# Performance work log

Measured on AMD Instinct MI355X. Metric: run time of the kernel, lower is better.

The kernel has to match this reference:

```python
import jax, jax.numpy as jnp
import numpy as np

NUM_USERS = 100000
NUM_ITEMS = 50000
EMBED_DIM = 128
NNZ = 2000000
N_LAYERS = 3


def setup_inputs() -> dict:
    key = jax.random.key(0)
    k1, k2, k3, k4, k5 = jax.random.split(key, 5)
    stdv = 1.0 / np.sqrt(EMBED_DIM)
    user_pref = jax.random.uniform(k1, (NUM_USERS, EMBED_DIM), jnp.float32, -stdv, stdv)
    item_pref = jax.random.uniform(k2, (NUM_ITEMS, EMBED_DIM), jnp.float32, -stdv, stdv)
    vals = jax.random.uniform(k3, (NNZ,), jnp.float32)
    rows = jax.random.randint(k4, (NNZ,), 0, NUM_USERS, jnp.int32)
    cols = jax.random.randint(k5, (NNZ,), 0, NUM_ITEMS, jnp.int32)
    return {"user_pref": user_pref, "item_pref": item_pref, "vals": vals,
            "rows": rows, "cols": cols}


def _spmm(vals, src_idx, dst_idx, x, num_out):
    # y[dst] += vals * x[src]  — SpMM over COO edge list
    msgs = vals[:, None] * x[src_idx]            # [nnz, D]
    return jax.ops.segment_sum(msgs, dst_idx, num_segments=num_out)


def reference(user_pref, item_pref, vals, rows, cols):
    u, it = user_pref, item_pref
    u_sum, i_sum = user_pref, item_pref
    for _ in range(N_LAYERS):
        # u_next = Graph @ item_layer ; i_next = Graph.T @ user_layer (same layer index)
        u_next = _spmm(vals, cols, rows, it, NUM_USERS)   # [U, D]
        i_next = _spmm(vals, rows, cols, u, NUM_ITEMS)    # [I, D]
        u, it = u_next, i_next
        u_sum = u_sum + u
        i_sum = i_sum + it
    inv = 1.0 / (N_LAYERS + 1)
    return (u_sum * inv, i_sum * inv)
```

## Files before the change

### kernel.cpp

```cpp
#include <hip/hip_runtime.h>


#define NUM_USERS 100000
#define NUM_ITEMS 50000
#define EMBED_DIM 128
#define NNZ_COUNT 2000000
#define NBUCK_U 391
#define NBUCK_I 196
#define EPB 8192
#define NBLK 245

typedef float v2f __attribute__((ext_vector_type(2)));


__device__ __forceinline__ unsigned bf16_rnd(float f) {
    unsigned u = __float_as_uint(f);
    return (u + 0x7FFFu + ((u >> 16) & 1u)) >> 16;
}
__device__ __forceinline__ unsigned pack_bf16(float x, float y) {
    return bf16_rnd(x) | (bf16_rnd(y) << 16);
}

__global__ __launch_bounds__(256) void to_bf16_dual(
    const float* __restrict__ a, unsigned* __restrict__ oa, int na8,
    const float* __restrict__ b, unsigned* __restrict__ ob, int nb8)
{
    int i = blockIdx.x * 256 + threadIdx.x;
    const float4* s4; uint4* d4;
    if (i < na8) {
        s4 = reinterpret_cast<const float4*>(a) + i * 2;
        d4 = reinterpret_cast<uint4*>(oa) + i;
    } else {
        i -= na8;
        if (i >= nb8) return;
        s4 = reinterpret_cast<const float4*>(b) + i * 2;
        d4 = reinterpret_cast<uint4*>(ob) + i;
    }
    float4 x = s4[0], y = s4[1];
    uint4 r;
    r.x = pack_bf16(x.x, x.y); r.y = pack_bf16(x.z, x.w);
    r.z = pack_bf16(y.x, y.y); r.w = pack_bf16(y.z, y.w);
    *d4 = r;
}


__global__ __launch_bounds__(256) void msplit_hist(
    const int* __restrict__ rows, const int* __restrict__ cols,
    int* __restrict__ hist_u, int* __restrict__ hist_i)
{
    __shared__ int h[NBUCK_U + NBUCK_I];
    for (int i = threadIdx.x; i < NBUCK_U + NBUCK_I; i += 256) h[i] = 0;
    __syncthreads();
    const int base = blockIdx.x * EPB;
    const int end = min(base + EPB, NNZ_COUNT);
    for (int e = base + threadIdx.x; e < end; e += 256) {
        atomicAdd(&h[rows[e] >> 8], 1);
        atomicAdd(&h[NBUCK_U + (cols[e] >> 8)], 1);
    }
    __syncthreads();
    for (int b = threadIdx.x; b < NBUCK_U; b += 256)
        hist_u[b * NBLK + blockIdx.x] = h[b];
    for (int b = threadIdx.x; b < NBUCK_I; b += 256)
        hist_i[b * NBLK + blockIdx.x] = h[NBUCK_U + b];
}

__global__ __launch_bounds__(256) void msplit_offsets(
    const int* __restrict__ hist_u, const int* __restrict__ hist_i,
    int* __restrict__ offs_u, int* __restrict__ offs_i,
    int* __restrict__ tot_u, int* __restrict__ tot_i)
{
    __shared__ int buf[256];
    int b = blockIdx.x;
    const int* hist; int* offs; int* tot; int nbuck;
    if (b < NBUCK_U) { hist = hist_u; offs = offs_u; tot = tot_u; nbuck = NBUCK_U; }
    else { b -= NBUCK_U; hist = hist_i; offs = offs_i; tot = tot_i; nbuck = NBUCK_I; }
    const int t = threadIdx.x;
    const int x = (t < NBLK) ? hist[b * NBLK + t] : 0;
    buf[t] = x;
    __syncthreads();
    for (int d = 1; d < 256; d <<= 1) {
        const int y = (t >= d) ? buf[t - d] : 0;
        __syncthreads();
        buf[t] += y;
        __syncthreads();
    }
    if (t < NBLK) offs[t * nbuck + b] = buf[t] - x;
    if (t == 255) tot[b] = buf[255];
}

__global__ __launch_bounds__(512) void scan_buckets(
    const int* __restrict__ tot_u, int* __restrict__ bbase_u,
    const int* __restrict__ tot_i, int* __restrict__ bbase_i)
{
    __shared__ int buf[512];
    const int t = threadIdx.x;
    const int* tot; int* bbase; int nb;
    if (blockIdx.x == 0) { tot = tot_u; bbase = bbase_u; nb = NBUCK_U; }
    else                 { tot = tot_i; bbase = bbase_i; nb = NBUCK_I; }
    const int v = (t < nb) ? tot[t] : 0;
    buf[t] = v;
    __syncthreads();
    for (int d = 1; d < 512; d <<= 1) {
        const int y = (t >= d) ? buf[t - d] : 0;
        __syncthreads();
        buf[t] += y;
        __syncthreads();
    }
    if (t <= nb) bbase[t] = buf[t] - v;
}

__global__ __launch_bounds__(256) void msplit_scatter(
    const int* __restrict__ rows, const int* __restrict__ cols,
    const float* __restrict__ vals,
    const int* __restrict__ offs_u, const int* __restrict__ offs_i,
    const int* __restrict__ bbase_u, const int* __restrict__ bbase_i,
    int2* __restrict__ stage_u, int2* __restrict__ stage_i)
{
    __shared__ int cu[NBUCK_U];
    __shared__ int ci[NBUCK_I];
    const int t = threadIdx.x;
    for (int b = t; b < NBUCK_U; b += 256)
        cu[b] = offs_u[blockIdx.x * NBUCK_U + b] + bbase_u[b];
    for (int b = t; b < NBUCK_I; b += 256)
        ci[b] = offs_i[blockIdx.x * NBUCK_I + b] + bbase_i[b];
    __syncthreads();
    const int base = blockIdx.x * EPB;
    const int end = min(base + EPB, NNZ_COUNT);
    for (int e = base + t; e < end; e += 256) {
        const int r = rows[e];
        const int c = cols[e];
        const int vb = __float_as_int(vals[e]);
        const int su = atomicAdd(&cu[r >> 8], 1);
        stage_u[su] = make_int2(c | ((r & 255) << 16), vb);
        const int si = atomicAdd(&ci[c >> 8], 1);
        stage_i[si] = make_int2(r | ((c & 255) << 17), vb);
    }
}

__global__ __launch_bounds__(256) void bucket_build(
    const int* __restrict__ bbase_u, const int2* __restrict__ stage_u,
    unsigned* __restrict__ pairs_u, int* __restrict__ ptr_u,
    const int* __restrict__ bbase_i, const int2* __restrict__ stage_i,
    unsigned* __restrict__ pairs_i, int* __restrict__ ptr_i)
{
    __shared__ int hcnt[256];
    __shared__ int buf[256];
    __shared__ int cur[256];
    const int t = threadIdx.x;
    int b = blockIdx.x;
    const bool uside = (b < NBUCK_U);
    const int* bbase; const int2* stage; unsigned* pairs; int* ptr; int n; int sh;
    if (uside) { bbase = bbase_u; stage = stage_u; pairs = pairs_u; ptr = ptr_u; n = NUM_USERS; sh = 16; }
    else { b -= NBUCK_U; bbase = bbase_i; stage = stage_i; pairs = pairs_i; ptr = ptr_i; n = NUM_ITEMS; sh = 17; }
    const int beg = bbase[b];
    const int end = bbase[b + 1];

    hcnt[t] = 0;
    __syncthreads();
    for (int idx = beg + t; idx < end; idx += 256)
        atomicAdd(&hcnt[(stage[idx].x >> sh) & 255], 1);
    __syncthreads();

    const int v = hcnt[t];
    buf[t] = v;
    __syncthreads();
    for (int d = 1; d < 256; d <<= 1) {
        const int y = (t >= d) ? buf[t - d] : 0;
        __syncthreads();
        buf[t] += y;
        __syncthreads();
    }
    const int rowbase = beg + buf[t] - v;
    cur[t] = rowbase;
    const int first = b << 8;
    if (first + t < n) ptr[first + t] = rowbase;
    if (first + t == n) ptr[n] = end;
    else if (first + 256 == n && t == 0) ptr[n] = end;
    __syncthreads();

    for (int idx = beg + t; idx < end; idx += 256) {
        const int2 s = stage[idx];
        const int local = (s.x >> sh) & 255;
        const unsigned vb = bf16_rnd(__int_as_float(s.y));
        unsigned packed;
        if (uside) packed = (unsigned)(s.x & 0xFFFF) | (vb << 16);
        else       packed = (unsigned)(s.x & 0x1FFFF) | ((vb & 0x7FFFu) << 17);
        const int slot = atomicAdd(&cur[local], 1);
        pairs[slot] = packed;
    }
}


template<bool USIDE>
__device__ __forceinline__ void decode_pair(unsigned s, int& c, float& v) {
    if (USIDE) { c = (int)(s & 0xFFFFu);  v = __uint_as_float(s & 0xFFFF0000u); }
    else       { c = (int)(s & 0x1FFFFu); v = __uint_as_float((s & 0xFFFE0000u) >> 1); }
}

template<int MODE, bool USIDE>
__device__ __forceinline__ void spmm_row_bf(
    const int* __restrict__ ptr, const unsigned* __restrict__ pairs,
    const unsigned* __restrict__ src, unsigned* __restrict__ dst,
    const unsigned* __restrict__ l1, const unsigned* __restrict__ l2,
    const float* __restrict__ base, float* __restrict__ out,
    int row, int lane)
{
    const int start = __builtin_amdgcn_readfirstlane(ptr[row]);
    const int end   = __builtin_amdgcn_readfirstlane(ptr[row + 1]);
    const unsigned* __restrict__ srcl = src + lane;
    v2f acc; acc.x = 0.f; acc.y = 0.f;

    int e = start;
    for (; e + 16 <= end; e += 16) {
        unsigned s[16]; int c[16]; float v[16]; unsigned g[16];
        #pragma unroll
        for (int k = 0; k < 16; ++k) s[k] = pairs[e + k];
        #pragma unroll
        for (int k = 0; k < 16; ++k) {
            decode_pair<USIDE>(s[k], c[k], v[k]);
            g[k] = srcl[(size_t)c[k] * 64];
        }
        #pragma unroll
        for (int k = 0; k < 16; ++k) {
            v2f gv; gv.x = __uint_as_float(g[k] << 16);
            gv.y = __uint_as_float(g[k] & 0xFFFF0000u);
            acc += v[k] * gv;
        }
    }
    for (; e + 8 <= end; e += 8) {
        unsigned s[8]; int c[8]; float v[8]; unsigned g[8];
        #pragma unroll
        for (int k = 0; k < 8; ++k) s[k] = pairs[e + k];
        #pragma unroll
        for (int k = 0; k < 8; ++k) {
            decode_pair<USIDE>(s[k], c[k], v[k]);
            g[k] = srcl[(size_t)c[k] * 64];
        }
        #pragma unroll
        for (int k = 0; k < 8; ++k) {
            v2f gv; gv.x = __uint_as_float(g[k] << 16);
            gv.y = __uint_as_float(g[k] & 0xFFFF0000u);
            acc += v[k] * gv;
        }
    }
    for (; e < end; ++e) {
        const unsigned s = pairs[e];
        int c; float v;
        decode_pair<USIDE>(s, c, v);
        const unsigned g = srcl[(size_t)c * 64];
        v2f gv; gv.x = __uint_as_float(g << 16);
        gv.y = __uint_as_float(g & 0xFFFF0000u);
        acc += v * gv;
    }

    if (MODE == 0) {
        __builtin_nontemporal_store(pack_bf16(acc.x, acc.y),
                                    dst + (size_t)row * 64 + lane);
    } else {
        const unsigned a1 = __builtin_nontemporal_load(l1 + (size_t)row * 64 + lane);
        const unsigned a2 = __builtin_nontemporal_load(l2 + (size_t)row * 64 + lane);
        const size_t o = (size_t)row * EMBED_DIM + (lane << 1);
        const v2f bs = __builtin_nontemporal_load(
            reinterpret_cast<const v2f*>(base + o));
        v2f r;
        r.x = (bs.x + __uint_as_float(a1 << 16) + __uint_as_float(a2 << 16) + acc.x) * 0.25f;
        r.y = (bs.y + __uint_as_float(a1 & 0xFFFF0000u) + __uint_as_float(a2 & 0xFFFF0000u) + acc.y) * 0.25f;
        __builtin_nontemporal_store(r, reinterpret_cast<v2f*>(out + o));
    }
}

template<int MODE>
__global__ __launch_bounds__(256) void csr_spmm_dual_bf(
    const int* __restrict__ ptr_u, const unsigned* __restrict__ pairs_u,
    const unsigned* __restrict__ src_u, unsigned* __restrict__ dst_u,
    const unsigned* __restrict__ l1_u, const unsigned* __restrict__ l2_u,
    const float* __restrict__ base_u, float* __restrict__ out_u,
    const int* __restrict__ ptr_i, const unsigned* __restrict__ pairs_i,
    const unsigned* __restrict__ src_i, unsigned* __restrict__ dst_i,
    const unsigned* __restrict__ l1_i, const unsigned* __restrict__ l2_i,
    const float* __restrict__ base_i, float* __restrict__ out_i,
    int GU)
{
    const int lane = threadIdx.x & 63;
    const int w = threadIdx.x >> 6;
    if ((int)blockIdx.x < GU) {
        const int row = blockIdx.x * 4 + w;
        if (row < NUM_USERS)
            spmm_row_bf<MODE, true>(ptr_u, pairs_u, src_u, dst_u, l1_u, l2_u, base_u, out_u, row, lane);
    } else {
        const int row = ((int)blockIdx.x - GU) * 4 + w;
        if (row < NUM_ITEMS)
            spmm_row_bf<MODE, false>(ptr_i, pairs_i, src_i, dst_i, l1_i, l2_i, base_i, out_i, row, lane);
    }
}


__global__ __launch_bounds__(256) void edge_spmm(
    const float* __restrict__ vals, const int* __restrict__ rows,
    const int* __restrict__ cols, const float* __restrict__ u_src,
    const float* __restrict__ i_src, float* __restrict__ u_dst,
    float* __restrict__ i_dst, int nnz)
{
    const int lane = threadIdx.x & 31;
    const int e = blockIdx.x * 8 + (threadIdx.x >> 5);
    if (e >= nnz) return;
    const float v = vals[e];
    const size_t ro = (size_t)rows[e] * EMBED_DIM + lane * 4;
    const size_t co = (size_t)cols[e] * EMBED_DIM + lane * 4;
    const float4 iv = *reinterpret_cast<const float4*>(i_src + co);
    const float4 uv = *reinterpret_cast<const float4*>(u_src + ro);
    atomicAdd(u_dst + ro + 0, v * iv.x); atomicAdd(u_dst + ro + 1, v * iv.y);
    atomicAdd(u_dst + ro + 2, v * iv.z); atomicAdd(u_dst + ro + 3, v * iv.w);
    atomicAdd(i_dst + co + 0, v * uv.x); atomicAdd(i_dst + co + 1, v * uv.y);
    atomicAdd(i_dst + co + 2, v * uv.z); atomicAdd(i_dst + co + 3, v * uv.w);
}

__global__ __launch_bounds__(256) void acc_scale(
    float* __restrict__ out, const float* __restrict__ x, long n, float scale)
{
    long i = ((long)blockIdx.x * blockDim.x + threadIdx.x) * 4;
    if (i >= n) return;
    float4 o = *reinterpret_cast<float4*>(out + i);
    float4 a = *reinterpret_cast<const float4*>(x + i);
    o.x = (o.x + a.x) * scale; o.y = (o.y + a.y) * scale;
    o.z = (o.z + a.z) * scale; o.w = (o.w + a.w) * scale;
    *reinterpret_cast<float4*>(out + i) = o;
}


extern "C" void kernel_launch(void* const* d_in, const int* in_sizes, int n_in,
                              void* d_out, int out_size, void* d_ws, size_t ws_size,
                              hipStream_t stream)
{
    const float* user = (const float*)d_in[0];
    const float* item = (const float*)d_in[1];
    const float* vals = (const float*)d_in[2];
    const int*   rows = (const int*)d_in[3];
    const int*   cols = (const int*)d_in[4];

    const size_t UD = (size_t)NUM_USERS * EMBED_DIM;
    const size_t ID = (size_t)NUM_ITEMS * EMBED_DIM;

    float* out_u = (float*)d_out;
    float* out_i = out_u + UD;

    char* ws = (char*)d_ws;
    unsigned* user_bf = (unsigned*)ws;              ws += UD * 2;
    unsigned* item_bf = (unsigned*)ws;              ws += ID * 2;
    unsigned* uA = (unsigned*)ws;                   ws += UD * 2;
    unsigned* uB = (unsigned*)ws;                   ws += UD * 2;
    unsigned* iA = (unsigned*)ws;                   ws += ID * 2;
    unsigned* iB = (unsigned*)ws;                   ws += ID * 2;
    unsigned* pairs_u = (unsigned*)ws;              ws += (size_t)NNZ_COUNT * 4;
    unsigned* pairs_i = (unsigned*)ws;              ws += (size_t)NNZ_COUNT * 4;
    int2* stage_u = (int2*)ws;                      ws += (size_t)NNZ_COUNT * 8;
    int2* stage_i = (int2*)ws;                      ws += (size_t)NNZ_COUNT * 8;
    int* ptr_u = (int*)ws;                          ws += (NUM_USERS + 1) * 4;
    int* ptr_i = (int*)ws;                          ws += (NUM_ITEMS + 1) * 4;
    int* bbase_u = (int*)ws;                        ws += (NBUCK_U + 1) * 4;
    int* bbase_i = (int*)ws;                        ws += (NBUCK_I + 1) * 4;
    const size_t REQ = (size_t)(ws - (char*)d_ws);

    int* hist_u = (int*)pairs_u;
    int* hist_i = hist_u + NBUCK_U * NBLK;
    int* offs_u = hist_i + NBUCK_I * NBLK;
    int* offs_i = offs_u + NBLK * NBUCK_U;
    int* tot_u  = offs_i + NBLK * NBUCK_I;
    int* tot_i  = tot_u + NBUCK_U;

    if (ws_size >= REQ) {
        const int NA8 = (int)(UD / 8), NB8 = (int)(ID / 8);
        to_bf16_dual<<<(NA8 + NB8 + 255) / 256, 256, 0, stream>>>(
            user, user_bf, NA8, item, item_bf, NB8);

        msplit_hist<<<NBLK, 256, 0, stream>>>(rows, cols, hist_u, hist_i);
        msplit_offsets<<<NBUCK_U + NBUCK_I, 256, 0, stream>>>(
            hist_u, hist_i, offs_u, offs_i, tot_u, tot_i);
        scan_buckets<<<2, 512, 0, stream>>>(tot_u, bbase_u, tot_i, bbase_i);
        msplit_scatter<<<NBLK, 256, 0, stream>>>(
            rows, cols, vals, offs_u, offs_i, bbase_u, bbase_i, stage_u, stage_i);
        bucket_build<<<NBUCK_U + NBUCK_I, 256, 0, stream>>>(
            bbase_u, stage_u, pairs_u, ptr_u,
            bbase_i, stage_i, pairs_i, ptr_i);

        const int GU = (NUM_USERS + 3) / 4;
        const int GI = (NUM_ITEMS + 3) / 4;

        csr_spmm_dual_bf<0><<<GU + GI, 256, 0, stream>>>(
            ptr_u, pairs_u, item_bf, uA, nullptr, nullptr, nullptr, nullptr,
            ptr_i, pairs_i, user_bf, iA, nullptr, nullptr, nullptr, nullptr, GU);
        csr_spmm_dual_bf<0><<<GU + GI, 256, 0, stream>>>(
            ptr_u, pairs_u, iA, uB, nullptr, nullptr, nullptr, nullptr,
            ptr_i, pairs_i, uA, iB, nullptr, nullptr, nullptr, nullptr, GU);
        csr_spmm_dual_bf<1><<<GU + GI, 256, 0, stream>>>(
            ptr_u, pairs_u, iB, nullptr, uA, uB, user, out_u,
            ptr_i, pairs_i, uB, nullptr, iA, iB, item, out_i, GU);
    } else {
        char* fw = (char*)d_ws;
        float* fuA = (float*)fw;                    fw += UD * 4;
        float* fuB = (float*)fw;                    fw += UD * 4;
        float* fiA = (float*)fw;                    fw += ID * 4;
        float* fiB = (float*)fw;                    fw += ID * 4;

        const int EDGE_BLOCKS = (NNZ_COUNT + 7) / 8;
        const int ACC_U = (int)(UD / 1024), ACC_I = (int)(ID / 1024);

        hipMemcpyAsync(out_u, user, UD * 4, hipMemcpyDeviceToDevice, stream);
        hipMemcpyAsync(out_i, item, ID * 4, hipMemcpyDeviceToDevice, stream);

        hipMemsetAsync(fuA, 0, UD * 4, stream);
        hipMemsetAsync(fiA, 0, ID * 4, stream);
        edge_spmm<<<EDGE_BLOCKS, 256, 0, stream>>>(vals, rows, cols, user, item, fuA, fiA, NNZ_COUNT);
        acc_scale<<<ACC_U, 256, 0, stream>>>(out_u, fuA, (long)UD, 1.0f);
        acc_scale<<<ACC_I, 256, 0, stream>>>(out_i, fiA, (long)ID, 1.0f);

        hipMemsetAsync(fuB, 0, UD * 4, stream);
        hipMemsetAsync(fiB, 0, ID * 4, stream);
        edge_spmm<<<EDGE_BLOCKS, 256, 0, stream>>>(vals, rows, cols, fuA, fiA, fuB, fiB, NNZ_COUNT);
        acc_scale<<<ACC_U, 256, 0, stream>>>(out_u, fuB, (long)UD, 1.0f);
        acc_scale<<<ACC_I, 256, 0, stream>>>(out_i, fiB, (long)ID, 1.0f);

        hipMemsetAsync(fuA, 0, UD * 4, stream);
        hipMemsetAsync(fiA, 0, ID * 4, stream);
        edge_spmm<<<EDGE_BLOCKS, 256, 0, stream>>>(vals, rows, cols, fuB, fiB, fuA, fiA, NNZ_COUNT);
        acc_scale<<<ACC_U, 256, 0, stream>>>(out_u, fuA, (long)UD, 0.25f);
        acc_scale<<<ACC_I, 256, 0, stream>>>(out_i, fiA, (long)ID, 0.25f);
    }
}
```

Before: 639.7 us.

## Stage scatter and bucket build through LDS for coalesced global writes

The multisplit scatter now sorts each block's edges by bucket in shared memory before writing them out, so writes to the staging arrays form contiguous runs instead of one random write per edge. The block size is halved to 4096 edges (489 blocks) and the offset scan is widened to 512 threads to match. bucket_build likewise assembles each bucket's packed pairs in an LDS buffer and writes them out contiguously when the bucket fits in BCAP entries, otherwise it falls back to direct scatter. This costs extra shared memory, more barriers, and a second pass over rows/cols per side. Preprocessing is only part of the total time, so the effect is bounded.

```diff
diff --git a/kernel.cpp b/kernel.cpp
--- a/kernel.cpp
+++ b/kernel.cpp
@@ -7,8 +7,9 @@
 #define NNZ_COUNT 2000000
 #define NBUCK_U 391
 #define NBUCK_I 196
-#define EPB 8192
-#define NBLK 245
+#define EPB 4096
+#define NBLK 489
+#define BCAP 12288
 
 typedef float v2f __attribute__((ext_vector_type(2)));
 
@@ -64,12 +65,12 @@
         hist_i[b * NBLK + blockIdx.x] = h[NBUCK_U + b];
 }
 
-__global__ __launch_bounds__(256) void msplit_offsets(
+__global__ __launch_bounds__(512) void msplit_offsets(
     const int* __restrict__ hist_u, const int* __restrict__ hist_i,
     int* __restrict__ offs_u, int* __restrict__ offs_i,
     int* __restrict__ tot_u, int* __restrict__ tot_i)
 {
-    __shared__ int buf[256];
+    __shared__ int buf[512];
     int b = blockIdx.x;
     const int* hist; int* offs; int* tot; int nbuck;
     if (b < NBUCK_U) { hist = hist_u; offs = offs_u; tot = tot_u; nbuck = NBUCK_U; }
@@ -78,14 +79,14 @@
     const int x = (t < NBLK) ? hist[b * NBLK + t] : 0;
     buf[t] = x;
     __syncthreads();
-    for (int d = 1; d < 256; d <<= 1) {
+    for (int d = 1; d < 512; d <<= 1) {
         const int y = (t >= d) ? buf[t - d] : 0;
         __syncthreads();
         buf[t] += y;
         __syncthreads();
     }
     if (t < NBLK) offs[t * nbuck + b] = buf[t] - x;
-    if (t == 255) tot[b] = buf[255];
+    if (t == 511) tot[b] = buf[511];
 }
 
 __global__ __launch_bounds__(512) void scan_buckets(
@@ -109,32 +110,95 @@
     if (t <= nb) bbase[t] = buf[t] - v;
 }
 
-__global__ __launch_bounds__(256) void msplit_scatter(
+__global__ __launch_bounds__(512) void msplit_scatter(
     const int* __restrict__ rows, const int* __restrict__ cols,
     const float* __restrict__ vals,
     const int* __restrict__ offs_u, const int* __restrict__ offs_i,
     const int* __restrict__ bbase_u, const int* __restrict__ bbase_i,
     int2* __restrict__ stage_u, int2* __restrict__ stage_i)
 {
-    __shared__ int cu[NBUCK_U];
-    __shared__ int ci[NBUCK_I];
+    __shared__ int buf[512];
+    __shared__ int cur[512];
+    __shared__ int gb[512];
+    __shared__ int ed0[EPB], ed1[EPB];
+    __shared__ unsigned short bpos[EPB];
     const int t = threadIdx.x;
-    for (int b = t; b < NBUCK_U; b += 256)
-        cu[b] = offs_u[blockIdx.x * NBUCK_U + b] + bbase_u[b];
-    for (int b = t; b < NBUCK_I; b += 256)
-        ci[b] = offs_i[blockIdx.x * NBUCK_I + b] + bbase_i[b];
-    __syncthreads();
     const int base = blockIdx.x * EPB;
     const int end = min(base + EPB, NNZ_COUNT);
-    for (int e = base + t; e < end; e += 256) {
+    const int n = end - base;
+
+    buf[t] = 0;
+    __syncthreads();
+    for (int e = base + t; e < end; e += 512)
+        atomicAdd(&buf[rows[e] >> 8], 1);
+    __syncthreads();
+    int x = buf[t];
+    __syncthreads();
+    {
+        buf[t] = x;
+        __syncthreads();
+        for (int d = 1; d < 512; d <<= 1) {
+            const int y = (t >= d) ? buf[t - d] : 0;
+            __syncthreads();
+            buf[t] += y;
+            __syncthreads();
+        }
+    }
+    {
+        const int excl = buf[t] - x;
+        cur[t] = excl;
+        if (t < NBUCK_U)
+            gb[t] = offs_u[blockIdx.x * NBUCK_U + t] + bbase_u[t] - excl;
+    }
+    __syncthreads();
+    for (int e = base + t; e < end; e += 512) {
         const int r = rows[e];
+        const int b = r >> 8;
+        const int pos = atomicAdd(&cur[b], 1);
+        ed0[pos] = cols[e] | ((r & 255) << 16);
+        ed1[pos] = __float_as_int(vals[e]);
+        bpos[pos] = (unsigned short)b;
+    }
+    __syncthreads();
+    for (int k = t; k < n; k += 512)
+        stage_u[gb[bpos[k]] + k] = make_int2(ed0[k], ed1[k]);
+    __syncthreads();
+
+    buf[t] = 0;
+    __syncthreads();
+    for (int e = base + t; e < end; e += 512)
+        atomicAdd(&buf[cols[e] >> 8], 1);
+    __syncthreads();
+    x = buf[t];
+    __syncthreads();
+    {
+        buf[t] = x;
+        __syncthreads();
+        for (int d = 1; d < 512; d <<= 1) {
+            const int y = (t >= d) ? buf[t - d] : 0;
+            __syncthreads();
+            buf[t] += y;
+            __syncthreads();
+        }
+    }
+    {
+        const int excl = buf[t] - x;
+        cur[t] = excl;
+        if (t < NBUCK_I)
+            gb[t] = offs_i[blockIdx.x * NBUCK_I + t] + bbase_i[t] - excl;
+    }
+    __syncthreads();
+    for (int e = base + t; e < end; e += 512) {
         const int c = cols[e];
-        const int vb = __float_as_int(vals[e]);
-        const int su = atomicAdd(&cu[r >> 8], 1);
-        stage_u[su] = make_int2(c | ((r & 255) << 16), vb);
-        const int si = atomicAdd(&ci[c >> 8], 1);
-        stage_i[si] = make_int2(r | ((c & 255) << 17), vb);
-    }
+        const int b = c >> 8;
+        const int pos = atomicAdd(&cur[b], 1);
+        ed0[pos] = rows[e] | ((c & 255) << 17);
+        ed1[pos] = __float_as_int(vals[e]);
+        bpos[pos] = (unsigned short)b;
+    }
+    __syncthreads();
+    for (int k = t; k < n; k += 512)
+        stage_i[gb[bpos[k]] + k] = make_int2(ed0[k], ed1[k]);
 }
 
 __global__ __launch_bounds__(256) void bucket_build(
@@ -146,6 +210,7 @@
     __shared__ int hcnt[256];
     __shared__ int buf[256];
     __shared__ int cur[256];
+    __shared__ unsigned plds[BCAP];
     const int t = threadIdx.x;
     int b = blockIdx.x;
     const bool uside = (b < NBUCK_U);
@@ -154,6 +219,7 @@
     else { b -= NBUCK_U; bbase = bbase_i; stage = stage_i; pairs = pairs_i; ptr = ptr_i; n = NUM_ITEMS; sh = 17; }
     const int beg = bbase[b];
     const int end = bbase[b + 1];
+    const int cnt = end - beg;
 
     hcnt[t] = 0;
     __syncthreads();
@@ -170,23 +236,42 @@
         buf[t] += y;
         __syncthreads();
     }
-    const int rowbase = beg + buf[t] - v;
-    cur[t] = rowbase;
+    const int excl = buf[t] - v;
+    const int rowbase = beg + excl;
     const int first = b << 8;
     if (first + t < n) ptr[first + t] = rowbase;
     if (first + t == n) ptr[n] = end;
     else if (first + 256 == n && t == 0) ptr[n] = end;
-    __syncthreads();
-
-    for (int idx = beg + t; idx < end; idx += 256) {
-        const int2 s = stage[idx];
-        const int local = (s.x >> sh) & 255;
-        const unsigned vb = bf16_rnd(__int_as_float(s.y));
-        unsigned packed;
-        if (uside) packed = (unsigned)(s.x & 0xFFFF) | (vb << 16);
-        else       packed = (unsigned)(s.x & 0x1FFFF) | ((vb & 0x7FFFu) << 17);
-        const int slot = atomicAdd(&cur[local], 1);
-        pairs[slot] = packed;
+
+    if (cnt <= BCAP) {
+        cur[t] = excl;
+        __syncthreads();
+        for (int idx = beg + t; idx < end; idx += 256) {
+            const int2 s = stage[idx];
+            const int local = (s.x >> sh) & 255;
+            const unsigned vb = bf16_rnd(__int_as_float(s.y));
+            unsigned packed;
+            if (uside) packed = (unsigned)(s.x & 0xFFFF) | (vb << 16);
+            else       packed = (unsigned)(s.x & 0x1FFFF) | ((vb & 0x7FFFu) << 17);
+            const int slot = atomicAdd(&cur[local], 1);
+            plds[slot] = packed;
+        }
+        __syncthreads();
+        for (int k = t; k < cnt; k += 256)
+            pairs[beg + k] = plds[k];
+    } else {
+        cur[t] = rowbase;
+        __syncthreads();
+        for (int idx = beg + t; idx < end; idx += 256) {
+            const int2 s = stage[idx];
+            const int local = (s.x >> sh) & 255;
+            const unsigned vb = bf16_rnd(__int_as_float(s.y));
+            unsigned packed;
+            if (uside) packed = (unsigned)(s.x & 0xFFFF) | (vb << 16);
+            else       packed = (unsigned)(s.x & 0x1FFFF) | ((vb & 0x7FFFu) << 17);
+            const int slot = atomicAdd(&cur[local], 1);
+            pairs[slot] = packed;
+        }
     }
 }
 
@@ -374,10 +459,10 @@
             user, user_bf, NA8, item, item_bf, NB8);
 
         msplit_hist<<<NBLK, 256, 0, stream>>>(rows, cols, hist_u, hist_i);
-        msplit_offsets<<<NBUCK_U + NBUCK_I, 256, 0, stream>>>(
+        msplit_offsets<<<NBUCK_U + NBUCK_I, 512, 0, stream>>>(
             hist_u, hist_i, offs_u, offs_i, tot_u, tot_i);
         scan_buckets<<<2, 512, 0, stream>>>(tot_u, bbase_u, tot_i, bbase_i);
-        msplit_scatter<<<NBLK, 256, 0, stream>>>(
+        msplit_scatter<<<NBLK, 512, 0, stream>>>(
             rows, cols, vals, offs_u, offs_i, bbase_u, bbase_i, stage_u, stage_i);
         bucket_build<<<NBUCK_U + NBUCK_I, 256, 0, stream>>>(
             bbase_u, stage_u, pairs_u, ptr_u,
```

After: 600.6 us. 6.1% less time.
